# Optimization experiments

Hardware: AMD Instinct MI355X
Metric: run time of the kernel (lower is better)

The kernel has to match this reference:

```python
import jax, jax.numpy as jnp
import numpy as np

PI = 3.141592653589793


def setup_inputs() -> dict:
    key = jax.random.key(0)
    ks = jax.random.split(key, 6)
    N, M, D, H = 2048, 512, 2, 128
    inp = {
        "input": jax.random.uniform(ks[0], (N, D), dtype=jnp.float32),
        "quad_x": jax.random.uniform(ks[1], (M, D), dtype=jnp.float32),
        "eq_param": jax.random.uniform(ks[2], (1,), dtype=jnp.float32),
        "W1": jax.random.normal(ks[3], (2 * D, H), dtype=jnp.float32) / np.sqrt(2 * D),
        "b1": jnp.zeros((H,), dtype=jnp.float32),
        "W2": jax.random.normal(ks[4], (H, H), dtype=jnp.float32) / np.sqrt(H),
        "b2": jnp.zeros((H,), dtype=jnp.float32),
        "W3": jax.random.normal(ks[5], (H, 1), dtype=jnp.float32) / np.sqrt(H),
        "b3": jnp.zeros((1,), dtype=jnp.float32),
    }
    return inp


def reference(input, quad_x, eq_param, W1, b1, W2, b2, W3, b3):
    # r_func: separable sinusoidal source weight per quadrature point -> [M]
    y = jnp.prod(jnp.sin(PI * eq_param * quad_x), axis=1)
    N, D = input.shape
    M = quad_x.shape[0]
    # batched concat over all (i, j) pairs: [N, M, 2D]
    pairs = jnp.concatenate(
        [jnp.broadcast_to(input[:, None, :], (N, M, D)),
         jnp.broadcast_to(quad_x[None, :, :], (N, M, D))], axis=-1)
    h = jnp.tanh(pairs @ W1 + b1)          # [N, M, H]
    h = jnp.tanh(h @ W2 + b2)              # [N, M, H]
    g = (h @ W3 + b3)[..., 0]              # [N, M] scalar mlp output per pair
    out = jnp.sum(g * y[None, :], axis=1, keepdims=True)  # quadrature-weighted sum -> [N, 1]
    return out
```

## Files before the change

kernel.cpp:

```cpp
#include <hip/hip_runtime.h>
#include <hip/hip_bf16.h>


using short8 = __attribute__((ext_vector_type(8))) short;
using f32x4  = __attribute__((ext_vector_type(4))) float;

#define N_IN   2048
#define M_Q    512
#define H_DIM  128
#define JC     16
#define JCHUNK 32

#define WS_A_OFF     0x000000u
#define WS_B_OFF     0x100000u
#define WS_Y_OFF     0x140000u
#define WS_SUMY_OFF  0x140800u
#define WS_W2T_OFF   0x141000u
#define WS_SP_OFF    0x150000u

#define PI_F   3.14159265358979323846f
#define TSCALE 2.885390081777927f

__device__ __forceinline__ float tanh_pre(float xs) {
    float t = __builtin_amdgcn_exp2f(xs);
    float r = __builtin_amdgcn_rcpf(1.0f + t);
    return __builtin_fmaf(-2.0f, r, 1.0f);
}

__device__ __forceinline__ unsigned short bf16b(float f) {
    __hip_bfloat16 h = __float2bfloat16(f);
    unsigned short u;
    __builtin_memcpy(&u, &h, 2);
    return u;
}

__device__ __forceinline__ void conv8(const float4& a0, const float4& a1,
                                      const float4& b0, const float4& b1,
                                      short8& dst) {
    dst[0] = (short)bf16b(tanh_pre(a0.x + b0.x));
    dst[1] = (short)bf16b(tanh_pre(a0.y + b0.y));
    dst[2] = (short)bf16b(tanh_pre(a0.z + b0.z));
    dst[3] = (short)bf16b(tanh_pre(a0.w + b0.w));
    dst[4] = (short)bf16b(tanh_pre(a1.x + b1.x));
    dst[5] = (short)bf16b(tanh_pre(a1.y + b1.y));
    dst[6] = (short)bf16b(tanh_pre(a1.z + b1.z));
    dst[7] = (short)bf16b(tanh_pre(a1.w + b1.w));
}

__global__ void k_pre(const float* __restrict__ input, const float* __restrict__ qx,
                      const float* __restrict__ eq, const float* __restrict__ W1,
                      const float* __restrict__ b1, const float* __restrict__ W2,
                      float* __restrict__ ws) {
    int b = blockIdx.x, t = threadIdx.x;
    float* A = ws + (WS_A_OFF >> 2);
    float* B = ws + (WS_B_OFF >> 2);
    float* Y = ws + (WS_Y_OFF >> 2);
    unsigned short* W2T = (unsigned short*)((char*)ws + WS_W2T_OFF);

    if (b < 1024) {
        int idx = b * 256 + t;
        int i = idx >> 7, h = idx & 127;
        A[idx] = TSCALE * (input[2 * i] * W1[h] + input[2 * i + 1] * W1[128 + h]);
    } else if (b < 1280) {
        int idx = (b - 1024) * 256 + t;
        int j = idx >> 7, h = idx & 127;
        B[idx] = TSCALE * (qx[2 * j] * W1[256 + h] + qx[2 * j + 1] * W1[384 + h] + b1[h]);
    } else if (b < 1344) {
        int idx = (b - 1280) * 256 + t;
        int n = idx >> 7, k = idx & 127;
        W2T[idx] = bf16b(TSCALE * W2[k * 128 + n]);
    } else {
        float e = eq[0];
        float s = 0.f;
        for (int rep = 0; rep < 2; ++rep) {
            int j = t + rep * 256;
            float yv = sinf(PI_F * e * qx[2 * j]) * sinf(PI_F * e * qx[2 * j + 1]);
            Y[j] = yv;
            s += yv;
        }
        __shared__ float red[4];
        for (int off = 32; off; off >>= 1) s += __shfl_down(s, off);
        if ((t & 63) == 0) red[t >> 6] = s;
        __syncthreads();
        if (t == 0) ws[WS_SUMY_OFF >> 2] = red[0] + red[1] + red[2] + red[3];
    }
}

__global__ __launch_bounds__(256, 2)
void k_main(const float* __restrict__ A, const float* __restrict__ B,
            const float* __restrict__ Y, const unsigned short* __restrict__ W2T,
            const float* __restrict__ b2, const float* __restrict__ W3,
            float* __restrict__ Sp) {
    __shared__ float Bs[JCHUNK * 128];
    __shared__ float ys[JCHUNK];
    __shared__ unsigned short xbuf[2 * 2 * 4 * 2 * 512];

    int t = threadIdx.x;
    int wave = t >> 6, lane = t & 63;
    int l16 = lane & 15, lg = lane >> 4;
    int ih = wave >> 1, p = wave & 1;
    int ibW = blockIdx.x * 64 + ih * 32;
    int jbase = blockIdx.y * JCHUNK;
    int myk0 = 2 * p;
    int otk0 = 2 * (1 - p);

    for (int off4 = t; off4 < (JCHUNK * 128) >> 2; off4 += 256)
        *(float4*)&Bs[off4 * 4] = *(const float4*)&B[jbase * 128 + off4 * 4];
    if (t < JCHUNK) ys[t] = Y[jbase + t];

    float4 aa[2][2][2];
#pragma unroll
    for (int rb = 0; rb < 2; ++rb)
#pragma unroll
        for (int kco = 0; kco < 2; ++kco) {
            const float* pa = &A[(ibW + rb * 16 + l16) * 128 + (myk0 + kco) * 32 + lg * 8];
            aa[rb][kco][0] = *(const float4*)pa;
            aa[rb][kco][1] = *(const float4*)(pa + 4);
        }

    short8 wfo[4][2], wfx[4][2];
#pragma unroll
    for (int nb = 0; nb < 4; ++nb)
#pragma unroll
        for (int kco = 0; kco < 2; ++kco) {
            int nrow = (p * 64 + nb * 16 + l16) * 128 + lg * 8;
            wfo[nb][kco] = *(const short8*)&W2T[nrow + (myk0 + kco) * 32];
            wfx[nb][kco] = *(const short8*)&W2T[nrow + (otk0 + kco) * 32];
        }

    float b2v[4], w3v[4];
#pragma unroll
    for (int nb = 0; nb < 4; ++nb) {
        b2v[nb] = TSCALE * b2[p * 64 + nb * 16 + l16];
        w3v[nb] = W3[p * 64 + nb * 16 + l16];
    }

    unsigned short* xw = xbuf + (ih * 4 + myk0) * 2 * 512 + lane * 8;
    unsigned short* xr = xbuf + (ih * 4 + otk0) * 2 * 512 + lane * 8;

    __syncthreads();

    f32x4 acc[2][4] = {};

#pragma unroll 1
    for (int jj = 0; jj < JCHUNK; ++jj) {
        int bsel = (jj & 1) * 8192;

        short8 av[2][2];
#pragma unroll
        for (int kco = 0; kco < 2; ++kco) {
            const float* bp = &Bs[jj * 128 + (myk0 + kco) * 32 + lg * 8];
            float4 bj0 = *(const float4*)bp;
            float4 bj1 = *(const float4*)(bp + 4);
#pragma unroll
            for (int rb = 0; rb < 2; ++rb)
                conv8(aa[rb][kco][0], aa[rb][kco][1], bj0, bj1, av[kco][rb]);
        }

#pragma unroll
        for (int kco = 0; kco < 2; ++kco)
#pragma unroll
            for (int rb = 0; rb < 2; ++rb)
                *(short8*)(xw + bsel + (kco * 2 + rb) * 512) = av[kco][rb];

        __syncthreads();

        short8 avx[2][2];
#pragma unroll
        for (int kco = 0; kco < 2; ++kco)
#pragma unroll
            for (int rb = 0; rb < 2; ++rb)
                avx[kco][rb] = *(const short8*)(xr + bsel + (kco * 2 + rb) * 512);

        f32x4 o[2][4];
#pragma unroll
        for (int rb = 0; rb < 2; ++rb)
#pragma unroll
            for (int nb = 0; nb < 4; ++nb) {
                o[rb][nb][0] = b2v[nb]; o[rb][nb][1] = b2v[nb];
                o[rb][nb][2] = b2v[nb]; o[rb][nb][3] = b2v[nb];
            }
#pragma unroll
        for (int kco = 0; kco < 2; ++kco)
#pragma unroll
            for (int rb = 0; rb < 2; ++rb)
#pragma unroll
                for (int nb = 0; nb < 4; ++nb)
                    o[rb][nb] = __builtin_amdgcn_mfma_f32_16x16x32_bf16(
                        av[kco][rb], wfo[nb][kco], o[rb][nb], 0, 0, 0);
#pragma unroll
        for (int kco = 0; kco < 2; ++kco)
#pragma unroll
            for (int rb = 0; rb < 2; ++rb)
#pragma unroll
                for (int nb = 0; nb < 4; ++nb)
                    o[rb][nb] = __builtin_amdgcn_mfma_f32_16x16x32_bf16(
                        avx[kco][rb], wfx[nb][kco], o[rb][nb], 0, 0, 0);

        float yj = ys[jj];
#pragma unroll
        for (int rb = 0; rb < 2; ++rb)
#pragma unroll
            for (int nb = 0; nb < 4; ++nb)
#pragma unroll
                for (int r = 0; r < 4; ++r)
                    acc[rb][nb][r] = __builtin_fmaf(yj, tanh_pre(o[rb][nb][r]),
                                                    acc[rb][nb][r]);
    }

    float s[2][4];
#pragma unroll
    for (int rb = 0; rb < 2; ++rb)
#pragma unroll
        for (int r = 0; r < 4; ++r) {
            float v = 0.f;
#pragma unroll
            for (int nb = 0; nb < 4; ++nb)
                v = __builtin_fmaf(acc[rb][nb][r], w3v[nb], v);
            s[rb][r] = v;
        }
#pragma unroll
    for (int m = 1; m < 16; m <<= 1)
#pragma unroll
        for (int rb = 0; rb < 2; ++rb)
#pragma unroll
            for (int r = 0; r < 4; ++r)
                s[rb][r] += __shfl_xor(s[rb][r], m);

    if (l16 == 0) {
        float* dst = Sp + (blockIdx.y * 2 + p) * N_IN;
#pragma unroll
        for (int rb = 0; rb < 2; ++rb)
#pragma unroll
            for (int r = 0; r < 4; ++r)
                dst[ibW + rb * 16 + lg * 4 + r] = s[rb][r];
    }
}

__global__ void k_fin(const float* __restrict__ Sp, const float* __restrict__ b3,
                      const float* __restrict__ ws, float* __restrict__ out) {
    int i = blockIdx.x * 256 + threadIdx.x;
    float acc = b3[0] * ws[WS_SUMY_OFF >> 2];
#pragma unroll
    for (int s = 0; s < 2 * JC; ++s) acc += Sp[s * N_IN + i];
    out[i] = acc;
}

extern "C" void kernel_launch(void* const* d_in, const int* in_sizes, int n_in,
                              void* d_out, int out_size, void* d_ws, size_t ws_size,
                              hipStream_t stream) {
    const float* input = (const float*)d_in[0];
    const float* qx    = (const float*)d_in[1];
    const float* eq    = (const float*)d_in[2];
    const float* W1    = (const float*)d_in[3];
    const float* b1    = (const float*)d_in[4];
    const float* W2    = (const float*)d_in[5];
    const float* b2    = (const float*)d_in[6];
    const float* W3    = (const float*)d_in[7];
    const float* b3    = (const float*)d_in[8];
    float* out = (float*)d_out;
    float* ws  = (float*)d_ws;

    const float* A = ws + (WS_A_OFF >> 2);
    const float* B = ws + (WS_B_OFF >> 2);
    const float* Y = ws + (WS_Y_OFF >> 2);
    const unsigned short* W2T = (const unsigned short*)((char*)d_ws + WS_W2T_OFF);
    float* Sp = (float*)((char*)d_ws + WS_SP_OFF);

    k_pre<<<1345, 256, 0, stream>>>(input, qx, eq, W1, b1, W2, ws);
    k_main<<<dim3(32, JC), 256, 0, stream>>>(A, B, Y, W2T, b2, W3, Sp);
    k_fin<<<8, 256, 0, stream>>>(Sp, b3, ws, out);
}
```

Baseline: 83.06 us.

## Switch to fp16 MFMA with packed conversion, fewer accumulators, more j-blocks

Replaces the bf16 activations and weights with fp16, using packed round-toward-zero conversion (cvt_pkrtz) in place of per-element bf16 rounding, and calls the f16 MFMA instruction. The per-j accumulation now applies the W3 dot product inside the loop, so 8 scalar sums replace 32 accumulator registers. The j-chunk is halved so twice as many blocks launch, and the precompute kernel is merged into 257 blocks that each do several elements. Together these aim to cut conversion ALU work, register pressure and launch imbalance, at the cost of more partial sums for the final reduction and fp16 range and precision behaviour.

```diff
diff --git a/kernel.cpp b/kernel.cpp
--- a/kernel.cpp
+++ b/kernel.cpp
@@ -1,15 +1,17 @@
 #include <hip/hip_runtime.h>
 #include <hip/hip_bf16.h>
-
-
-using short8 = __attribute__((ext_vector_type(8))) short;
+#include <hip/hip_fp16.h>
+
+
+using fp16x2 = __attribute__((ext_vector_type(2))) __fp16;
+using half8  = __attribute__((ext_vector_type(8))) _Float16;
 using f32x4  = __attribute__((ext_vector_type(4))) float;
 
 #define N_IN   2048
 #define M_Q    512
 #define H_DIM  128
-#define JC     16
-#define JCHUNK 32
+#define JC     32
+#define JCHUNK 16
 
 #define WS_A_OFF     0x000000u
 #define WS_B_OFF     0x100000u
@@ -27,24 +29,19 @@
     return __builtin_fmaf(-2.0f, r, 1.0f);
 }
 
-__device__ __forceinline__ unsigned short bf16b(float f) {
-    __hip_bfloat16 h = __float2bfloat16(f);
-    unsigned short u;
-    __builtin_memcpy(&u, &h, 2);
-    return u;
-}
-
 __device__ __forceinline__ void conv8(const float4& a0, const float4& a1,
                                       const float4& b0, const float4& b1,
-                                      short8& dst) {
-    dst[0] = (short)bf16b(tanh_pre(a0.x + b0.x));
-    dst[1] = (short)bf16b(tanh_pre(a0.y + b0.y));
-    dst[2] = (short)bf16b(tanh_pre(a0.z + b0.z));
-    dst[3] = (short)bf16b(tanh_pre(a0.w + b0.w));
-    dst[4] = (short)bf16b(tanh_pre(a1.x + b1.x));
-    dst[5] = (short)bf16b(tanh_pre(a1.y + b1.y));
-    dst[6] = (short)bf16b(tanh_pre(a1.z + b1.z));
-    dst[7] = (short)bf16b(tanh_pre(a1.w + b1.w));
+                                      half8& dst) {
+    float t0 = tanh_pre(a0.x + b0.x), t1 = tanh_pre(a0.y + b0.y);
+    float t2 = tanh_pre(a0.z + b0.z), t3 = tanh_pre(a0.w + b0.w);
+    float t4 = tanh_pre(a1.x + b1.x), t5 = tanh_pre(a1.y + b1.y);
+    float t6 = tanh_pre(a1.z + b1.z), t7 = tanh_pre(a1.w + b1.w);
+    fp16x2 p[4];
+    p[0] = __builtin_amdgcn_cvt_pkrtz(t0, t1);
+    p[1] = __builtin_amdgcn_cvt_pkrtz(t2, t3);
+    p[2] = __builtin_amdgcn_cvt_pkrtz(t4, t5);
+    p[3] = __builtin_amdgcn_cvt_pkrtz(t6, t7);
+    __builtin_memcpy(&dst, p, 16);
 }
 
 __global__ void k_pre(const float* __restrict__ input, const float* __restrict__ qx,
@@ -55,23 +52,28 @@
     float* A = ws + (WS_A_OFF >> 2);
     float* B = ws + (WS_B_OFF >> 2);
     float* Y = ws + (WS_Y_OFF >> 2);
-    unsigned short* W2T = (unsigned short*)((char*)ws + WS_W2T_OFF);
-
-    if (b < 1024) {
-        int idx = b * 256 + t;
-        int i = idx >> 7, h = idx & 127;
-        A[idx] = TSCALE * (input[2 * i] * W1[h] + input[2 * i + 1] * W1[128 + h]);
-    } else if (b < 1280) {
-        int idx = (b - 1024) * 256 + t;
-        int j = idx >> 7, h = idx & 127;
-        B[idx] = TSCALE * (qx[2 * j] * W1[256 + h] + qx[2 * j + 1] * W1[384 + h] + b1[h]);
-    } else if (b < 1344) {
-        int idx = (b - 1280) * 256 + t;
-        int n = idx >> 7, k = idx & 127;
-        W2T[idx] = bf16b(TSCALE * W2[k * 128 + n]);
+    _Float16* W2T = (_Float16*)((char*)ws + WS_W2T_OFF);
+
+    if (b < 256) {
+        int u = b * 256 + t;
+#pragma unroll
+        for (int rep = 0; rep < 4; ++rep) {
+            int idx = u + rep * 65536;
+            int i = idx >> 7, h = idx & 127;
+            A[idx] = TSCALE * (input[2 * i] * W1[h] + input[2 * i + 1] * W1[128 + h]);
+        }
+        {
+            int j = u >> 7, h = u & 127;
+            B[u] = TSCALE * (qx[2 * j] * W1[256 + h] + qx[2 * j + 1] * W1[384 + h] + b1[h]);
+        }
+        if (u < 16384) {
+            int n = u >> 7, k = u & 127;
+            W2T[u] = (_Float16)(TSCALE * W2[k * 128 + n]);
+        }
     } else {
         float e = eq[0];
         float s = 0.f;
+#pragma unroll
         for (int rep = 0; rep < 2; ++rep) {
             int j = t + rep * 256;
             float yv = sinf(PI_F * e * qx[2 * j]) * sinf(PI_F * e * qx[2 * j + 1]);
@@ -88,12 +90,12 @@
 
 __global__ __launch_bounds__(256, 2)
 void k_main(const float* __restrict__ A, const float* __restrict__ B,
-            const float* __restrict__ Y, const unsigned short* __restrict__ W2T,
+            const float* __restrict__ Y, const _Float16* __restrict__ W2T,
             const float* __restrict__ b2, const float* __restrict__ W3,
             float* __restrict__ Sp) {
     __shared__ float Bs[JCHUNK * 128];
     __shared__ float ys[JCHUNK];
-    __shared__ unsigned short xbuf[2 * 2 * 4 * 2 * 512];
+    __shared__ _Float16 xbuf[2 * 2 * 4 * 2 * 512];
 
     int t = threadIdx.x;
     int wave = t >> 6, lane = t & 63;
@@ -118,14 +120,14 @@
             aa[rb][kco][1] = *(const float4*)(pa + 4);
         }
 
-    short8 wfo[4][2], wfx[4][2];
+    half8 wfo[4][2], wfx[4][2];
 #pragma unroll
     for (int nb = 0; nb < 4; ++nb)
 #pragma unroll
         for (int kco = 0; kco < 2; ++kco) {
             int nrow = (p * 64 + nb * 16 + l16) * 128 + lg * 8;
-            wfo[nb][kco] = *(const short8*)&W2T[nrow + (myk0 + kco) * 32];
-            wfx[nb][kco] = *(const short8*)&W2T[nrow + (otk0 + kco) * 32];
+            wfo[nb][kco] = *(const half8*)&W2T[nrow + (myk0 + kco) * 32];
+            wfx[nb][kco] = *(const half8*)&W2T[nrow + (otk0 + kco) * 32];
         }
 
     float b2v[4], w3v[4];
@@ -135,18 +137,18 @@
         w3v[nb] = W3[p * 64 + nb * 16 + l16];
     }
 
-    unsigned short* xw = xbuf + (ih * 4 + myk0) * 2 * 512 + lane * 8;
-    unsigned short* xr = xbuf + (ih * 4 + otk0) * 2 * 512 + lane * 8;
+    _Float16* xw = xbuf + (ih * 4 + myk0) * 2 * 512 + lane * 8;
+    _Float16* xr = xbuf + (ih * 4 + otk0) * 2 * 512 + lane * 8;
 
     __syncthreads();
 
-    f32x4 acc[2][4] = {};
+    float s[2][4] = {};
 
 #pragma unroll 1
     for (int jj = 0; jj < JCHUNK; ++jj) {
         int bsel = (jj & 1) * 8192;
 
-        short8 av[2][2];
+        half8 av[2][2];
 #pragma unroll
         for (int kco = 0; kco < 2; ++kco) {
             const float* bp = &Bs[jj * 128 + (myk0 + kco) * 32 + lg * 8];
@@ -161,16 +163,16 @@
         for (int kco = 0; kco < 2; ++kco)
 #pragma unroll
             for (int rb = 0; rb < 2; ++rb)
-                *(short8*)(xw + bsel + (kco * 2 + rb) * 512) = av[kco][rb];
+                *(half8*)(xw + bsel + (kco * 2 + rb) * 512) = av[kco][rb];
 
         __syncthreads();
 
-        short8 avx[2][2];
-#pragma unroll
-        for (int kco = 0; kco < 2; ++kco)
-#pragma unroll
-            for (int rb = 0; rb < 2; ++rb)
-                avx[kco][rb] = *(const short8*)(xr + bsel + (kco * 2 + rb) * 512);
+        half8 avx[2][2];
+#pragma unroll
+        for (int kco = 0; kco < 2; ++kco)
+#pragma unroll
+            for (int rb = 0; rb < 2; ++rb)
+                avx[kco][rb] = *(const half8*)(xr + bsel + (kco * 2 + rb) * 512);
 
         f32x4 o[2][4];
 #pragma unroll
@@ -186,7 +188,7 @@
             for (int rb = 0; rb < 2; ++rb)
 #pragma unroll
                 for (int nb = 0; nb < 4; ++nb)
-                    o[rb][nb] = __builtin_amdgcn_mfma_f32_16x16x32_bf16(
+                    o[rb][nb] = __builtin_amdgcn_mfma_f32_16x16x32_f16(
                         av[kco][rb], wfo[nb][kco], o[rb][nb], 0, 0, 0);
 #pragma unroll
         for (int kco = 0; kco < 2; ++kco)
@@ -194,31 +196,22 @@
             for (int rb = 0; rb < 2; ++rb)
 #pragma unroll
                 for (int nb = 0; nb < 4; ++nb)
-                    o[rb][nb] = __builtin_amdgcn_mfma_f32_16x16x32_bf16(
+                    o[rb][nb] = __builtin_amdgcn_mfma_f32_16x16x32_f16(
                         avx[kco][rb], wfx[nb][kco], o[rb][nb], 0, 0, 0);
 
         float yj = ys[jj];
 #pragma unroll
         for (int rb = 0; rb < 2; ++rb)
 #pragma unroll
-            for (int nb = 0; nb < 4; ++nb)
-#pragma unroll
-                for (int r = 0; r < 4; ++r)
-                    acc[rb][nb][r] = __builtin_fmaf(yj, tanh_pre(o[rb][nb][r]),
-                                                    acc[rb][nb][r]);
-    }
-
-    float s[2][4];
-#pragma unroll
-    for (int rb = 0; rb < 2; ++rb)
-#pragma unroll
-        for (int r = 0; r < 4; ++r) {
-            float v = 0.f;
-#pragma unroll
-            for (int nb = 0; nb < 4; ++nb)
-                v = __builtin_fmaf(acc[rb][nb][r], w3v[nb], v);
-            s[rb][r] = v;
-        }
+            for (int r = 0; r < 4; ++r) {
+                float v = 0.f;
+#pragma unroll
+                for (int nb = 0; nb < 4; ++nb)
+                    v = __builtin_fmaf(tanh_pre(o[rb][nb][r]), w3v[nb], v);
+                s[rb][r] = __builtin_fmaf(yj, v, s[rb][r]);
+            }
+    }
+
 #pragma unroll
     for (int m = 1; m < 16; m <<= 1)
 #pragma unroll
@@ -264,10 +257,10 @@
     const float* A = ws + (WS_A_OFF >> 2);
     const float* B = ws + (WS_B_OFF >> 2);
     const float* Y = ws + (WS_Y_OFF >> 2);
-    const unsigned short* W2T = (const unsigned short*)((char*)d_ws + WS_W2T_OFF);
+    const _Float16* W2T = (const _Float16*)((char*)d_ws + WS_W2T_OFF);
     float* Sp = (float*)((char*)d_ws + WS_SP_OFF);
 
-    k_pre<<<1345, 256, 0, stream>>>(input, qx, eq, W1, b1, W2, ws);
+    k_pre<<<257, 256, 0, stream>>>(input, qx, eq, W1, b1, W2, ws);
     k_main<<<dim3(32, JC), 256, 0, stream>>>(A, B, Y, W2T, b2, W3, Sp);
     k_fin<<<8, 256, 0, stream>>>(Sp, b3, ws, out);
 }
```

After: 96.16 us. +15.8%, slower.
